# Performance work log

Hardware: AMD Instinct MI355X
Metric: run time of the kernel (lower is better)

Reference implementation:

```python
import jax, jax.numpy as jnp
import numpy as np

H, W, NC, L = 768, 768, 1, 8
PROJ = L * (L + 1) // 2  # = l*(l-1)/2 + l = 36
LMBDA = 0.1
NU = 0.01
SIGMAP = 1.0 / (3.0 + L)
SIGMAS = 1.0
TAUU = 1.0 / 6.0
N_ITERS = 2  # two primal-dual iterations of run()'s hot loop


def _member_matrix():
    # M[z, K] = 1 iff level z lies in combination K=(k1,k2), k1<=z<=k2.
    # Equivalent to the precomputed k_indices lists in k_indices_for_mu().
    M = np.zeros((L, PROJ), dtype=np.float32)
    K = 0
    for k1 in range(L):
        for k2 in range(k1, L):
            M[k1:k2 + 1, K] = 1.0
            K += 1
    return jnp.asarray(M)

_M = _member_matrix()
_K_OVER_L = jnp.arange(1, L + 1, dtype=jnp.float32) / L  # k/l, k = 1..L


def _fwd_diff(x, axis):
    # torch.cat((torch.diff(x, dim=axis), zeros_like(last slice)), dim=axis)
    pad = [(0, 0)] * x.ndim
    pad[axis] = (0, 1)
    return jnp.pad(jnp.diff(x, axis=axis), pad)


def _div(p, axis):
    # Negative adjoint of _fwd_diff (backward difference with the last
    # slice of p treated as zero): (div p)_j = p_j - p_{j-1}.
    n = p.shape[axis]
    sl = [slice(None)] * p.ndim
    sl[axis] = slice(0, n - 1)
    zpad = [(0, 0)] * p.ndim
    zpad[axis] = (0, 1)
    p_eff = jnp.pad(p[tuple(sl)], zpad)
    spad = [(0, 0)] * p.ndim
    spad[axis] = (1, 0)
    sl2 = [slice(None)] * p.ndim
    sl2[axis] = slice(0, n)
    return p_eff - jnp.pad(p_eff, spad)[tuple(sl2)]


def _parabola(ubar, p1, p2, p3, mu1, mu2, f):
    u1 = _fwd_diff(ubar, 0)
    u2 = _fwd_diff(ubar, 1)
    u3 = _fwd_diff(ubar, 3)
    # level-wise gather-sum over combinations via membership matrix
    mu1sum = jnp.einsum('hwcp,zp->hwcz', mu1, _M)
    mu2sum = jnp.einsum('hwcp,zp->hwcz', mu2, _M)
    u1 = p1 + SIGMAP * (u1 + mu1sum)
    u2 = p2 + SIGMAP * (u2 + mu2sum)
    u3 = p3 + SIGMAP * u3
    quad = LMBDA * (_K_OVER_L - f[..., None]) ** 2      # [h,w,c,L]
    B = 0.25 * (u1 * u1 + u2 * u2) - quad
    mask = u3 < B
    # cubic-root solve projecting onto the parabola
    y = u3 + quad
    norm = jnp.sqrt(u1 * u1 + u2 * u2)
    a = 0.5 * norm                      # 2*0.25*norm
    b = (2.0 / 3.0) * (1.0 - 0.5 * y)   # 2/3*(1 - 2*0.25*y)
    sb = jnp.sqrt(jnp.maximum(-b, 0.0))
    d = jnp.where(b < 0, (a - sb ** 3) * (a + sb ** 3), a * a + b ** 3)
    sd = jnp.sqrt(jnp.maximum(d, 0.0))
    c = jnp.cbrt(a + sd)
    c_safe = jnp.where(c == 0, 1.0, c)
    sb3 = jnp.where(sb > 0, sb ** 3, 1.0)
    cosarg = jnp.clip(a / sb3, -1.0, 1.0)
    v_neg = 2.0 * sb * jnp.cos(jnp.arccos(cosarg) / 3.0)
    v = jnp.where((d >= 0) & (c == 0), 0.0,
                  jnp.where(d < 0, v_neg, c - b / c_safe))
    norm_safe = jnp.where(norm == 0, 1.0, norm)
    scale = (v / 0.5) / norm_safe       # v / (2*0.25) / norm
    p1n = jnp.where(mask, jnp.where(norm == 0, 0.0, scale * u1), u1)
    p2n = jnp.where(mask, jnp.where(norm == 0, 0.0, scale * u2), u2)
    p3n = jnp.where(mask, 0.25 * (p1n * p1n + p2n * p2n) - quad, u3)
    return p1n, p2n, p3n


def _l2projection(s1, s2, mubar1, mubar2):
    m1 = s1 - SIGMAS * mubar1
    m2 = s2 - SIGMAS * mubar2
    norm = jnp.sqrt(m1 * m1 + m2 * m2)
    mask = norm > NU
    ns = jnp.where(mask, norm, 1.0)
    return jnp.where(mask, m1 * NU / ns, m1), jnp.where(mask, m2 * NU / ns, m2)


def _mu(mu1, mu2, s1, s2, p1, p2):
    tau = 1.0 / (2.0 + PROJ / 4.0)
    # t[K] = sum of p over levels k1..k2 for combination K (same membership M)
    t1 = jnp.einsum('hwcz,zp->hwcp', p1, _M)
    t2 = jnp.einsum('hwcz,zp->hwcp', p2, _M)
    mu1n = mu1 + tau * (s1 - t1)
    mu2n = mu2 + tau * (s2 - t2)
    return mu1n, mu2n, 2.0 * mu1n - mu1, 2.0 * mu2n - mu2


def _clipping(u, p1, p2, p3):
    div = _div(p1, 0) + _div(p2, 1) + _div(p3, 3)
    un = jnp.clip(u + TAUU * div, 0.0, 1.0)
    return un, 2.0 * un - u


def setup_inputs() -> dict:
    key = jax.random.key(0)
    ks = jax.random.split(key, 12)
    lvl = (H, W, NC, L)
    prj = (H, W, NC, PROJ)
    return {
        'u': jax.random.uniform(ks[0], lvl, jnp.float32),
        'ubar': jax.random.uniform(ks[1], lvl, jnp.float32),
        'p1': jax.random.normal(ks[2], lvl, jnp.float32),
        'p2': jax.random.normal(ks[3], lvl, jnp.float32),
        'p3': jax.random.normal(ks[4], lvl, jnp.float32),
        's1': jax.random.normal(ks[5], prj, jnp.float32),
        's2': jax.random.normal(ks[6], prj, jnp.float32),
        'mu1': jax.random.normal(ks[7], prj, jnp.float32),
        'mu2': jax.random.normal(ks[8], prj, jnp.float32),
        'mubar1': jax.random.normal(ks[9], prj, jnp.float32),
        'mubar2': jax.random.normal(ks[10], prj, jnp.float32),
        'f': jax.random.uniform(ks[11], (H, W, NC), jnp.float32),
    }


def reference(u, ubar, p1, p2, p3, s1, s2, mu1, mu2, mubar1, mubar2, f):
    for _ in range(N_ITERS):
        p1, p2, p3 = _parabola(ubar, p1, p2, p3, mu1, mu2, f)
        s1, s2 = _l2projection(s1, s2, mubar1, mubar2)
        mu1, mu2, mubar1, mubar2 = _mu(mu1, mu2, s1, s2, p1, p2)
        u, ubar = _clipping(u, p1, p2, p3)
    return u
```

## Files before the change

kernel.cpp:

```cpp
#include <hip/hip_runtime.h>
#include <math.h>

#define HH   768
#define WW   768
#define LL   8
#define NPIX (HH*WW)
#define NLVL (NPIX*LL)
#define BLK  128
#define THR  512
#define REC  37

#define SIGMAP (1.0f/11.0f)
#define TAUMU  (1.0f/11.0f)
#define TAUU   (1.0f/6.0f)
#define LMBDA  0.1f
#define NUC    0.01f

__device__ __forceinline__ float4 ld4(const float* p){ return *reinterpret_cast<const float4*>(p); }
__device__ __forceinline__ void  st4(float* p, float4 v){ *reinterpret_cast<float4*>(p) = v; }
__device__ __forceinline__ float2 ld2(const float* p){ return *reinterpret_cast<const float2*>(p); }
__device__ __forceinline__ void  st2(float* p, float2 v){ *reinterpret_cast<float2*>(p) = v; }

__device__ __forceinline__ void parabola1(float u1, float u2, float u3, float quad,
                                          float& p1n, float& p2n, float& p3n)
{
  float nn = u1*u1 + u2*u2;
  float Bv = 0.25f*nn - quad;
  if (u3 < Bv) {
    float y    = u3 + quad;
    float norm = sqrtf(nn);
    float a    = 0.5f*norm;
    float b    = (2.0f/3.0f)*(1.0f - 0.5f*y);
    float sb   = sqrtf(fmaxf(-b, 0.0f));
    float sb3  = sb*sb*sb;
    float d    = (b < 0.0f) ? (a - sb3)*(a + sb3) : (a*a + b*b*b);
    float v;
    if (d < 0.0f) {
      float sb3s = (sb > 0.0f) ? sb3 : 1.0f;
      float ca   = fminf(fmaxf(a/sb3s, -1.0f), 1.0f);
      v = 2.0f*sb*cosf(acosf(ca)*(1.0f/3.0f));
    } else {
      float sd = sqrtf(d);
      float c  = cbrtf(a + sd);
      v = (c == 0.0f) ? 0.0f : (c - b/c);
    }
    float nsafe = (norm == 0.0f) ? 1.0f : norm;
    float scale = (v + v)/nsafe;
    p1n = (norm == 0.0f) ? 0.0f : scale*u1;
    p2n = (norm == 0.0f) ? 0.0f : scale*u2;
    p3n = 0.25f*(p1n*p1n + p2n*p2n) - quad;
  } else {
    p1n = u1; p2n = u2; p3n = u3;
  }
}

__device__ __forceinline__ void stage1_512(const float* __restrict__ g, float* __restrict__ lds, int tid)
{
  #pragma unroll
  for (int j = 0; j < 2; ++j) {
    int g4 = (tid + THR*j) * 4;
    float4 v = ld4(g + g4);
    int pl  = g4 / 36;
    int off = g4 - pl*36;
    float* d = lds + pl*REC + off;
    d[0]=v.x; d[1]=v.y; d[2]=v.z; d[3]=v.w;
  }
  if (tid < 128) {
    int g4 = (tid + 1024) * 4;
    float4 v = ld4(g + g4);
    int pl  = g4 / 36;
    int off = g4 - pl*36;
    float* d = lds + pl*REC + off;
    d[0]=v.x; d[1]=v.y; d[2]=v.z; d[3]=v.w;
  }
}

__device__ __forceinline__ void stage_diff_512(const float* __restrict__ ga, const float* __restrict__ gb,
                                               float* __restrict__ lds, int tid)
{
  #pragma unroll
  for (int j = 0; j < 2; ++j) {
    int g4 = (tid + THR*j) * 4;
    float4 a = ld4(ga + g4);
    float4 b = ld4(gb + g4);
    int pl  = g4 / 36;
    int off = g4 - pl*36;
    float* d = lds + pl*REC + off;
    d[0]=a.x-b.x; d[1]=a.y-b.y; d[2]=a.z-b.z; d[3]=a.w-b.w;
  }
  if (tid < 128) {
    int g4 = (tid + 1024) * 4;
    float4 a = ld4(ga + g4);
    float4 b = ld4(gb + g4);
    int pl  = g4 / 36;
    int off = g4 - pl*36;
    float* d = lds + pl*REC + off;
    d[0]=a.x-b.x; d[1]=a.y-b.y; d[2]=a.z-b.z; d[3]=a.w-b.w;
  }
}

template<int ZB>
__device__ __forceinline__ void memb_scan2(const float* __restrict__ rA, const float* __restrict__ rB,
                                           float (&ms1)[2], float (&ms2)[2])
{
  int K = 0;
  #pragma unroll
  for (int k1 = 0; k1 < 8; ++k1) {
    #pragma unroll
    for (int k2 = k1; k2 < 8; ++k2) {
      if (k2 >= ZB && k1 <= ZB + 1) {
        float v1 = rA[K], v2 = rB[K];
        #pragma unroll
        for (int z = (k1 > ZB ? k1 : ZB); z <= (k2 < ZB+1 ? k2 : ZB+1); ++z) {
          ms1[z-ZB] += v1; ms2[z-ZB] += v2;
        }
      }
      ++K;
    }
  }
}

template<int ZB>
__device__ __forceinline__ void proj_scan2(const float* __restrict__ rA, const float* __restrict__ rB,
                                           const float (&pre1)[9], const float (&pre2)[9],
                                           float (&A1)[2], float (&A2)[2])
{
  int K = 0;
  #pragma unroll
  for (int k1 = 0; k1 < 8; ++k1) {
    #pragma unroll
    for (int k2 = k1; k2 < 8; ++k2) {
      if (k2 >= ZB && k1 <= ZB + 1) {
        float m1 = rA[K], m2 = rB[K];
        float nrm = sqrtf(m1*m1 + m2*m2);
        float s1n, s2n;
        if (nrm > NUC) { float r = NUC/nrm; s1n = m1*r; s2n = m2*r; }
        else           { s1n = m1; s2n = m2; }
        float d1 = s1n - (pre1[k2+1] - pre1[k1]);
        float d2 = s2n - (pre2[k2+1] - pre2[k1]);
        #pragma unroll
        for (int z = (k1 > ZB ? k1 : ZB); z <= (k2 < ZB+1 ? k2 : ZB+1); ++z) {
          A1[z-ZB] += d1; A2[z-ZB] += d2;
        }
      }
      ++K;
    }
  }
}

__global__ __launch_bounds__(THR, 8) void k_iter1(
  const float* __restrict__ ubar, const float* __restrict__ p1,
  const float* __restrict__ p2,   const float* __restrict__ p3,
  const float* __restrict__ s1,   const float* __restrict__ s2,
  const float* __restrict__ mu1,  const float* __restrict__ mu2,
  const float* __restrict__ mb1,  const float* __restrict__ mb2,
  const float* __restrict__ f,
  float* __restrict__ op1, float* __restrict__ op2, float* __restrict__ op3,
  float* __restrict__ oms1, float* __restrict__ oms2)
{
  __shared__ float sA[BLK*REC];
  __shared__ float sB[BLK*REC];

  const int tid  = threadIdx.x;
  const int lpx  = tid & 127;
  const int hi   = tid >> 7;
  const int zb   = hi * 2;
  const int blk0 = blockIdx.x * BLK;
  const int p    = blk0 + lpx;
  const int w  = p % WW;
  const int h  = p / WW;
  const int pr = (w < WW-1) ? p+1  : p;
  const int pd = (h < HH-1) ? p+WW : p;

  stage1_512(mu1 + (size_t)blk0*36, sA, tid);
  stage1_512(mu2 + (size_t)blk0*36, sB, tid);
  __syncthreads();

  const float* rA = sA + lpx*REC;
  const float* rB = sB + lpx*REC;
  float ms1[2] = {0.f,0.f}, ms2[2] = {0.f,0.f};
  switch (hi) {
    case 0: memb_scan2<0>(rA, rB, ms1, ms2); break;
    case 1: memb_scan2<2>(rA, rB, ms1, ms2); break;
    case 2: memb_scan2<4>(rA, rB, ms1, ms2); break;
    default: memb_scan2<6>(rA, rB, ms1, ms2); break;
  }

  float2 ubq  = ld2(ubar + (size_t)p *8 + zb);
  float  ubx  = (zb < 6) ? ubar[(size_t)p*8 + zb + 2] : 0.f;
  float2 ubrq = ld2(ubar + (size_t)pr*8 + zb);
  float2 ubdq = ld2(ubar + (size_t)pd*8 + zb);
  float2 p1q  = ld2(p1 + (size_t)p*8 + zb);
  float2 p2q  = ld2(p2 + (size_t)p*8 + zb);
  float2 p3q  = ld2(p3 + (size_t)p*8 + zb);
  const float fv = f[p];

  float ubv[3]  = {ubq.x, ubq.y, ubx};
  float ubrv[2] = {ubrq.x, ubrq.y};
  float ubdv[2] = {ubdq.x, ubdq.y};
  float p1v[2]  = {p1q.x, p1q.y};
  float p2v[2]  = {p2q.x, p2q.y};
  float p3v[2]  = {p3q.x, p3q.y};

  float pn1[2], pn2[2], pn3[2];
  #pragma unroll
  for (int i = 0; i < 2; ++i) {
    int z = zb + i;
    float du1 = ubdv[i] - ubv[i];
    float du2 = ubrv[i] - ubv[i];
    float du3 = (z < 7) ? (ubv[i+1] - ubv[i]) : 0.f;
    float u1 = p1v[i] + SIGMAP*(du1 + ms1[i]);
    float u2 = p2v[i] + SIGMAP*(du2 + ms2[i]);
    float u3 = p3v[i] + SIGMAP*du3;
    float t  = (float)(z+1)*0.125f - fv;
    float quad = LMBDA*t*t;
    parabola1(u1,u2,u3,quad, pn1[i],pn2[i],pn3[i]);
  }
  st2(op1 + (size_t)p*8 + zb, make_float2(pn1[0],pn1[1]));
  st2(op2 + (size_t)p*8 + zb, make_float2(pn2[0],pn2[1]));
  st2(op3 + (size_t)p*8 + zb, make_float2(pn3[0],pn3[1]));

  __syncthreads();
  float* ex1 = sA;
  float* ex2 = sA + 8*BLK;
  #pragma unroll
  for (int i = 0; i < 2; ++i) {
    ex1[(zb+i)*BLK + lpx] = pn1[i];
    ex2[(zb+i)*BLK + lpx] = pn2[i];
  }
  __syncthreads();
  float pre1[9], pre2[9];
  pre1[0] = 0.f; pre2[0] = 0.f;
  #pragma unroll
  for (int z = 0; z < 8; ++z) {
    pre1[z+1] = pre1[z] + ex1[z*BLK + lpx];
    pre2[z+1] = pre2[z] + ex2[z*BLK + lpx];
  }

  __syncthreads();
  stage_diff_512(s1 + (size_t)blk0*36, mb1 + (size_t)blk0*36, sA, tid);
  stage_diff_512(s2 + (size_t)blk0*36, mb2 + (size_t)blk0*36, sB, tid);
  __syncthreads();

  float A1[2] = {0.f,0.f}, A2[2] = {0.f,0.f};
  switch (hi) {
    case 0: proj_scan2<0>(rA, rB, pre1, pre2, A1, A2); break;
    case 1: proj_scan2<2>(rA, rB, pre1, pre2, A1, A2); break;
    case 2: proj_scan2<4>(rA, rB, pre1, pre2, A1, A2); break;
    default: proj_scan2<6>(rA, rB, pre1, pre2, A1, A2); break;
  }

  st2(oms1 + (size_t)p*8 + zb,
      make_float2(ms1[0] + TAUMU*A1[0], ms1[1] + TAUMU*A1[1]));
  st2(oms2 + (size_t)p*8 + zb,
      make_float2(ms2[0] + TAUMU*A2[0], ms2[1] + TAUMU*A2[1]));
}

__global__ __launch_bounds__(256, 8) void k_parab2(
  const float* __restrict__ ubar,
  float* __restrict__ p1, float* __restrict__ p2, float* __restrict__ p3,
  const float* __restrict__ ms1g, const float* __restrict__ ms2g,
  const float* __restrict__ f)
{
  const int t  = blockIdx.x*blockDim.x + threadIdx.x;
  const int p  = t >> 1;
  const int hi = t & 1;
  const int zb = hi * 4;
  const int w  = p % WW;
  const int h  = p / WW;
  const int pr = (w < WW-1) ? p+1  : p;
  const int pd = (h < HH-1) ? p+WW : p;

  float4 ubq  = ld4(ubar + (size_t)p *8 + zb);
  float  ubx  = hi ? 0.f : ubar[(size_t)p*8 + 4];
  float4 ubrq = ld4(ubar + (size_t)pr*8 + zb);
  float4 ubdq = ld4(ubar + (size_t)pd*8 + zb);
  float4 p1q  = ld4(p1 + (size_t)p*8 + zb);
  float4 p2q  = ld4(p2 + (size_t)p*8 + zb);
  float4 p3q  = ld4(p3 + (size_t)p*8 + zb);
  float4 m1q  = ld4(ms1g + (size_t)p*8 + zb);
  float4 m2q  = ld4(ms2g + (size_t)p*8 + zb);
  const float fv = f[p];

  float ubv[5]  = {ubq.x, ubq.y, ubq.z, ubq.w, ubx};
  float ubrv[4] = {ubrq.x, ubrq.y, ubrq.z, ubrq.w};
  float ubdv[4] = {ubdq.x, ubdq.y, ubdq.z, ubdq.w};
  float p1v[4]  = {p1q.x, p1q.y, p1q.z, p1q.w};
  float p2v[4]  = {p2q.x, p2q.y, p2q.z, p2q.w};
  float p3v[4]  = {p3q.x, p3q.y, p3q.z, p3q.w};
  float ms1[4]  = {m1q.x, m1q.y, m1q.z, m1q.w};
  float ms2[4]  = {m2q.x, m2q.y, m2q.z, m2q.w};

  float pn1[4], pn2[4], pn3[4];
  #pragma unroll
  for (int i = 0; i < 4; ++i) {
    int z = zb + i;
    float du1 = ubdv[i] - ubv[i];
    float du2 = ubrv[i] - ubv[i];
    float du3 = (z < 7) ? (ubv[i+1] - ubv[i]) : 0.f;
    float u1 = p1v[i] + SIGMAP*(du1 + ms1[i]);
    float u2 = p2v[i] + SIGMAP*(du2 + ms2[i]);
    float u3 = p3v[i] + SIGMAP*du3;
    float tt = (float)(z+1)*0.125f - fv;
    float quad = LMBDA*tt*tt;
    parabola1(u1,u2,u3,quad, pn1[i],pn2[i],pn3[i]);
  }
  st4(p1 + (size_t)p*8 + zb, make_float4(pn1[0],pn1[1],pn1[2],pn1[3]));
  st4(p2 + (size_t)p*8 + zb, make_float4(pn2[0],pn2[1],pn2[2],pn2[3]));
  st4(p3 + (size_t)p*8 + zb, make_float4(pn3[0],pn3[1],pn3[2],pn3[3]));
}

__global__ __launch_bounds__(256, 8) void k_clip(
  const float* __restrict__ uin,
  const float* __restrict__ p1, const float* __restrict__ p2,
  const float* __restrict__ p3,
  float* __restrict__ uout, float* __restrict__ ubarout)
{
  const int t  = blockIdx.x*blockDim.x + threadIdx.x;
  const int p  = t >> 1;
  const int hi = t & 1;
  const int zb = hi * 4;
  const int w  = p % WW;
  const int h  = p / WW;
  const int pu = (h > 0) ? p-WW : p;
  const int pl = (w > 0) ? p-1  : p;

  float4 uq   = ld4(uin + (size_t)p *8 + zb);
  float4 a1q  = ld4(p1  + (size_t)p *8 + zb);
  float4 a1uq = ld4(p1  + (size_t)pu*8 + zb);
  float4 a2q  = ld4(p2  + (size_t)p *8 + zb);
  float4 a2lq = ld4(p2  + (size_t)pl*8 + zb);
  float4 a3q  = ld4(p3  + (size_t)p *8 + zb);
  float  a3m  = hi ? p3[(size_t)p*8 + 3] : 0.f;

  float uv[4]  = {uq.x, uq.y, uq.z, uq.w};
  float a1[4]  = {a1q.x, a1q.y, a1q.z, a1q.w};
  float a1u[4] = {a1uq.x, a1uq.y, a1uq.z, a1uq.w};
  float a2[4]  = {a2q.x, a2q.y, a2q.z, a2q.w};
  float a2l[4] = {a2lq.x, a2lq.y, a2lq.z, a2lq.w};
  float a3[4]  = {a3q.x, a3q.y, a3q.z, a3q.w};

  const float fh1 = (h < HH-1) ? 1.f : 0.f;
  const float fh0 = (h > 0)    ? 1.f : 0.f;
  const float fw1 = (w < WW-1) ? 1.f : 0.f;
  const float fw0 = (w > 0)    ? 1.f : 0.f;

  float un[4], ubn[4];
  #pragma unroll
  for (int i = 0; i < 4; ++i) {
    int z = zb + i;
    float d1 = fh1*a1[i] - fh0*a1u[i];
    float d2 = fw1*a2[i] - fw0*a2l[i];
    float upper = (z < 7) ? a3[i] : 0.f;
    float lower = (z > 0) ? ((i > 0) ? a3[i-1] : a3m) : 0.f;
    float d3 = upper - lower;
    float x  = uv[i] + TAUU*(d1+d2+d3);
    x = fminf(fmaxf(x, 0.f), 1.f);
    un[i]  = x;
    ubn[i] = 2.f*x - uv[i];
  }
  st4(uout + (size_t)p*8 + zb, make_float4(un[0],un[1],un[2],un[3]));
  if (ubarout) st4(ubarout + (size_t)p*8 + zb, make_float4(ubn[0],ubn[1],ubn[2],ubn[3]));
}

extern "C" void kernel_launch(void* const* d_in, const int* in_sizes, int n_in,
                              void* d_out, int out_size, void* d_ws, size_t ws_size,
                              hipStream_t stream)
{
  const float* u    = (const float*)d_in[0];
  const float* ubar = (const float*)d_in[1];
  const float* p1   = (const float*)d_in[2];
  const float* p2   = (const float*)d_in[3];
  const float* p3   = (const float*)d_in[4];
  const float* s1   = (const float*)d_in[5];
  const float* s2   = (const float*)d_in[6];
  const float* mu1  = (const float*)d_in[7];
  const float* mu2  = (const float*)d_in[8];
  const float* mb1  = (const float*)d_in[9];
  const float* mb2  = (const float*)d_in[10];
  const float* f    = (const float*)d_in[11];

  float* ws   = (float*)d_ws;
  float* wp1  = ws;
  float* wp2  = ws + 1*(size_t)NLVL;
  float* wp3  = ws + 2*(size_t)NLVL;
  float* wms1 = ws + 3*(size_t)NLVL;
  float* wms2 = ws + 4*(size_t)NLVL;
  float* wub  = ws + 5*(size_t)NLVL;
  float* uo   = (float*)d_out;

  k_iter1 <<<dim3(NPIX/BLK), dim3(THR), 0, stream>>>(
      ubar,p1,p2,p3,s1,s2,mu1,mu2,mb1,mb2,f, wp1,wp2,wp3,wms1,wms2);
  k_clip  <<<dim3(NPIX*2/256), dim3(256), 0, stream>>>(u, wp1,wp2,wp3, uo, wub);
  k_parab2<<<dim3(NPIX*2/256), dim3(256), 0, stream>>>(wub, wp1,wp2,wp3, wms1,wms2, f);
  k_clip  <<<dim3(NPIX*2/256), dim3(256), 0, stream>>>(uo, wp1,wp2,wp3, uo, nullptr);
}
```

Baseline: 627.8 us.

## Shrink k_iter1 blocks and time-share one LDS buffer across mu/s channels

Restructures k_iter1 from 128-pixel/512-thread blocks to 64-pixel/128-thread blocks, each thread handling 4 levels instead of 2. It uses a single LDS buffer reused sequentially for mu1 then mu2, and for the projected s1 then s2. The L2 projection of s onto the nu-ball moves into the staging step, so each combination's norm is computed while loading rather than during the scan. This cuts LDS use per block to raise occupancy. In exchange it loads s1/s2/mubar twice, recomputes the norm, and adds more barriers.

```diff
diff --git a/kernel.cpp b/kernel.cpp
--- a/kernel.cpp
+++ b/kernel.cpp
@@ -6,8 +6,8 @@
 #define LL   8
 #define NPIX (HH*WW)
 #define NLVL (NPIX*LL)
-#define BLK  128
-#define THR  512
+#define BLKI 64
+#define THRI 128
 #define REC  37
 
 #define SIGMAP (1.0f/11.0f)
@@ -18,8 +18,6 @@
 
 __device__ __forceinline__ float4 ld4(const float* p){ return *reinterpret_cast<const float4*>(p); }
 __device__ __forceinline__ void  st4(float* p, float4 v){ *reinterpret_cast<float4*>(p) = v; }
-__device__ __forceinline__ float2 ld2(const float* p){ return *reinterpret_cast<const float2*>(p); }
-__device__ __forceinline__ void  st2(float* p, float2 v){ *reinterpret_cast<float2*>(p) = v; }
 
 __device__ __forceinline__ void parabola1(float u1, float u2, float u3, float quad,
                                           float& p1n, float& p2n, float& p3n)
@@ -54,19 +52,19 @@
   }
 }
 
-__device__ __forceinline__ void stage1_512(const float* __restrict__ g, float* __restrict__ lds, int tid)
-{
-  #pragma unroll
-  for (int j = 0; j < 2; ++j) {
-    int g4 = (tid + THR*j) * 4;
+__device__ __forceinline__ void stage1_128(const float* __restrict__ g, float* __restrict__ lds, int tid)
+{
+  #pragma unroll
+  for (int j = 0; j < 4; ++j) {
+    int g4 = (tid + THRI*j) * 4;
     float4 v = ld4(g + g4);
     int pl  = g4 / 36;
     int off = g4 - pl*36;
     float* d = lds + pl*REC + off;
     d[0]=v.x; d[1]=v.y; d[2]=v.z; d[3]=v.w;
   }
-  if (tid < 128) {
-    int g4 = (tid + 1024) * 4;
+  if (tid < 64) {
+    int g4 = (tid + 512) * 4;
     float4 v = ld4(g + g4);
     int pl  = g4 / 36;
     int off = g4 - pl*36;
@@ -75,45 +73,60 @@
   }
 }
 
-__device__ __forceinline__ void stage_diff_512(const float* __restrict__ ga, const float* __restrict__ gb,
-                                               float* __restrict__ lds, int tid)
-{
-  #pragma unroll
-  for (int j = 0; j < 2; ++j) {
-    int g4 = (tid + THR*j) * 4;
-    float4 a = ld4(ga + g4);
-    float4 b = ld4(gb + g4);
+template<int SEL>
+__device__ __forceinline__ float celem(float m1, float m2)
+{
+  float nrm = sqrtf(m1*m1 + m2*m2);
+  float o = (SEL == 0) ? m1 : m2;
+  if (nrm > NUC) o = o * (NUC/nrm);
+  return o;
+}
+
+template<int SEL>
+__device__ __forceinline__ void stage_c(const float* __restrict__ ga1, const float* __restrict__ gb1,
+                                        const float* __restrict__ ga2, const float* __restrict__ gb2,
+                                        float* __restrict__ lds, int tid)
+{
+  #pragma unroll
+  for (int j = 0; j < 4; ++j) {
+    int g4 = (tid + THRI*j) * 4;
+    float4 a1 = ld4(ga1 + g4), b1 = ld4(gb1 + g4);
+    float4 a2 = ld4(ga2 + g4), b2 = ld4(gb2 + g4);
     int pl  = g4 / 36;
     int off = g4 - pl*36;
     float* d = lds + pl*REC + off;
-    d[0]=a.x-b.x; d[1]=a.y-b.y; d[2]=a.z-b.z; d[3]=a.w-b.w;
-  }
-  if (tid < 128) {
-    int g4 = (tid + 1024) * 4;
-    float4 a = ld4(ga + g4);
-    float4 b = ld4(gb + g4);
+    d[0] = celem<SEL>(a1.x-b1.x, a2.x-b2.x);
+    d[1] = celem<SEL>(a1.y-b1.y, a2.y-b2.y);
+    d[2] = celem<SEL>(a1.z-b1.z, a2.z-b2.z);
+    d[3] = celem<SEL>(a1.w-b1.w, a2.w-b2.w);
+  }
+  if (tid < 64) {
+    int g4 = (tid + 512) * 4;
+    float4 a1 = ld4(ga1 + g4), b1 = ld4(gb1 + g4);
+    float4 a2 = ld4(ga2 + g4), b2 = ld4(gb2 + g4);
     int pl  = g4 / 36;
     int off = g4 - pl*36;
     float* d = lds + pl*REC + off;
-    d[0]=a.x-b.x; d[1]=a.y-b.y; d[2]=a.z-b.z; d[3]=a.w-b.w;
+    d[0] = celem<SEL>(a1.x-b1.x, a2.x-b2.x);
+    d[1] = celem<SEL>(a1.y-b1.y, a2.y-b2.y);
+    d[2] = celem<SEL>(a1.z-b1.z, a2.z-b2.z);
+    d[3] = celem<SEL>(a1.w-b1.w, a2.w-b2.w);
   }
 }
 
 template<int ZB>
-__device__ __forceinline__ void memb_scan2(const float* __restrict__ rA, const float* __restrict__ rB,
-                                           float (&ms1)[2], float (&ms2)[2])
+__device__ __forceinline__ void memb_scan1(const float* __restrict__ r, float (&ms)[4])
 {
   int K = 0;
   #pragma unroll
   for (int k1 = 0; k1 < 8; ++k1) {
     #pragma unroll
     for (int k2 = k1; k2 < 8; ++k2) {
-      if (k2 >= ZB && k1 <= ZB + 1) {
-        float v1 = rA[K], v2 = rB[K];
+      if (k2 >= ZB && k1 < ZB + 4) {
+        float v = r[K];
         #pragma unroll
-        for (int z = (k1 > ZB ? k1 : ZB); z <= (k2 < ZB+1 ? k2 : ZB+1); ++z) {
-          ms1[z-ZB] += v1; ms2[z-ZB] += v2;
-        }
+        for (int z = (k1 > ZB ? k1 : ZB); z <= (k2 < ZB+3 ? k2 : ZB+3); ++z)
+          ms[z-ZB] += v;
       }
       ++K;
     }
@@ -121,34 +134,26 @@
 }
 
 template<int ZB>
-__device__ __forceinline__ void proj_scan2(const float* __restrict__ rA, const float* __restrict__ rB,
-                                           const float (&pre1)[9], const float (&pre2)[9],
-                                           float (&A1)[2], float (&A2)[2])
+__device__ __forceinline__ void projA_scan(const float* __restrict__ r, const float (&pre)[9],
+                                           float (&A)[4])
 {
   int K = 0;
   #pragma unroll
   for (int k1 = 0; k1 < 8; ++k1) {
     #pragma unroll
     for (int k2 = k1; k2 < 8; ++k2) {
-      if (k2 >= ZB && k1 <= ZB + 1) {
-        float m1 = rA[K], m2 = rB[K];
-        float nrm = sqrtf(m1*m1 + m2*m2);
-        float s1n, s2n;
-        if (nrm > NUC) { float r = NUC/nrm; s1n = m1*r; s2n = m2*r; }
-        else           { s1n = m1; s2n = m2; }
-        float d1 = s1n - (pre1[k2+1] - pre1[k1]);
-        float d2 = s2n - (pre2[k2+1] - pre2[k1]);
+      if (k2 >= ZB && k1 < ZB + 4) {
+        float d = r[K] - (pre[k2+1] - pre[k1]);
         #pragma unroll
-        for (int z = (k1 > ZB ? k1 : ZB); z <= (k2 < ZB+1 ? k2 : ZB+1); ++z) {
-          A1[z-ZB] += d1; A2[z-ZB] += d2;
-        }
+        for (int z = (k1 > ZB ? k1 : ZB); z <= (k2 < ZB+3 ? k2 : ZB+3); ++z)
+          A[z-ZB] += d;
       }
       ++K;
     }
   }
 }
 
-__global__ __launch_bounds__(THR, 8) void k_iter1(
+__global__ __launch_bounds__(THRI, 8) void k_iter1(
   const float* __restrict__ ubar, const float* __restrict__ p1,
   const float* __restrict__ p2,   const float* __restrict__ p3,
   const float* __restrict__ s1,   const float* __restrict__ s2,
@@ -158,53 +163,49 @@
   float* __restrict__ op1, float* __restrict__ op2, float* __restrict__ op3,
   float* __restrict__ oms1, float* __restrict__ oms2)
 {
-  __shared__ float sA[BLK*REC];
-  __shared__ float sB[BLK*REC];
+  __shared__ float sBuf[BLKI*REC];
 
   const int tid  = threadIdx.x;
-  const int lpx  = tid & 127;
-  const int hi   = tid >> 7;
-  const int zb   = hi * 2;
-  const int blk0 = blockIdx.x * BLK;
+  const int lpx  = tid & 63;
+  const int hi   = tid >> 6;
+  const int zb   = hi * 4;
+  const int blk0 = blockIdx.x * BLKI;
   const int p    = blk0 + lpx;
   const int w  = p % WW;
   const int h  = p / WW;
   const int pr = (w < WW-1) ? p+1  : p;
   const int pd = (h < HH-1) ? p+WW : p;
 
-  stage1_512(mu1 + (size_t)blk0*36, sA, tid);
-  stage1_512(mu2 + (size_t)blk0*36, sB, tid);
-  __syncthreads();
-
-  const float* rA = sA + lpx*REC;
-  const float* rB = sB + lpx*REC;
-  float ms1[2] = {0.f,0.f}, ms2[2] = {0.f,0.f};
-  switch (hi) {
-    case 0: memb_scan2<0>(rA, rB, ms1, ms2); break;
-    case 1: memb_scan2<2>(rA, rB, ms1, ms2); break;
-    case 2: memb_scan2<4>(rA, rB, ms1, ms2); break;
-    default: memb_scan2<6>(rA, rB, ms1, ms2); break;
-  }
-
-  float2 ubq  = ld2(ubar + (size_t)p *8 + zb);
-  float  ubx  = (zb < 6) ? ubar[(size_t)p*8 + zb + 2] : 0.f;
-  float2 ubrq = ld2(ubar + (size_t)pr*8 + zb);
-  float2 ubdq = ld2(ubar + (size_t)pd*8 + zb);
-  float2 p1q  = ld2(p1 + (size_t)p*8 + zb);
-  float2 p2q  = ld2(p2 + (size_t)p*8 + zb);
-  float2 p3q  = ld2(p3 + (size_t)p*8 + zb);
+  stage1_128(mu1 + (size_t)blk0*36, sBuf, tid);
+  __syncthreads();
+  const float* rC = sBuf + lpx*REC;
+  float ms1[4] = {0.f,0.f,0.f,0.f};
+  if (hi) memb_scan1<4>(rC, ms1); else memb_scan1<0>(rC, ms1);
+  __syncthreads();
+  stage1_128(mu2 + (size_t)blk0*36, sBuf, tid);
+  __syncthreads();
+  float ms2[4] = {0.f,0.f,0.f,0.f};
+  if (hi) memb_scan1<4>(rC, ms2); else memb_scan1<0>(rC, ms2);
+
+  float4 ubq  = ld4(ubar + (size_t)p *8 + zb);
+  float  ubx  = hi ? 0.f : ubar[(size_t)p*8 + 4];
+  float4 ubrq = ld4(ubar + (size_t)pr*8 + zb);
+  float4 ubdq = ld4(ubar + (size_t)pd*8 + zb);
+  float4 p1q  = ld4(p1 + (size_t)p*8 + zb);
+  float4 p2q  = ld4(p2 + (size_t)p*8 + zb);
+  float4 p3q  = ld4(p3 + (size_t)p*8 + zb);
   const float fv = f[p];
 
-  float ubv[3]  = {ubq.x, ubq.y, ubx};
-  float ubrv[2] = {ubrq.x, ubrq.y};
-  float ubdv[2] = {ubdq.x, ubdq.y};
-  float p1v[2]  = {p1q.x, p1q.y};
-  float p2v[2]  = {p2q.x, p2q.y};
-  float p3v[2]  = {p3q.x, p3q.y};
-
-  float pn1[2], pn2[2], pn3[2];
-  #pragma unroll
-  for (int i = 0; i < 2; ++i) {
+  float ubv[5]  = {ubq.x, ubq.y, ubq.z, ubq.w, ubx};
+  float ubrv[4] = {ubrq.x, ubrq.y, ubrq.z, ubrq.w};
+  float ubdv[4] = {ubdq.x, ubdq.y, ubdq.z, ubdq.w};
+  float p1v[4]  = {p1q.x, p1q.y, p1q.z, p1q.w};
+  float p2v[4]  = {p2q.x, p2q.y, p2q.z, p2q.w};
+  float p3v[4]  = {p3q.x, p3q.y, p3q.z, p3q.w};
+
+  float pn1[4], pn2[4], pn3[4];
+  #pragma unroll
+  for (int i = 0; i < 4; ++i) {
     int z = zb + i;
     float du1 = ubdv[i] - ubv[i];
     float du2 = ubrv[i] - ubv[i];
@@ -216,44 +217,46 @@
     float quad = LMBDA*t*t;
     parabola1(u1,u2,u3,quad, pn1[i],pn2[i],pn3[i]);
   }
-  st2(op1 + (size_t)p*8 + zb, make_float2(pn1[0],pn1[1]));
-  st2(op2 + (size_t)p*8 + zb, make_float2(pn2[0],pn2[1]));
-  st2(op3 + (size_t)p*8 + zb, make_float2(pn3[0],pn3[1]));
-
-  __syncthreads();
-  float* ex1 = sA;
-  float* ex2 = sA + 8*BLK;
-  #pragma unroll
-  for (int i = 0; i < 2; ++i) {
-    ex1[(zb+i)*BLK + lpx] = pn1[i];
-    ex2[(zb+i)*BLK + lpx] = pn2[i];
+  st4(op1 + (size_t)p*8 + zb, make_float4(pn1[0],pn1[1],pn1[2],pn1[3]));
+  st4(op2 + (size_t)p*8 + zb, make_float4(pn2[0],pn2[1],pn2[2],pn2[3]));
+  st4(op3 + (size_t)p*8 + zb, make_float4(pn3[0],pn3[1],pn3[2],pn3[3]));
+
+  __syncthreads();
+  float* ex1 = sBuf;
+  float* ex2 = sBuf + 8*BLKI;
+  #pragma unroll
+  for (int i = 0; i < 4; ++i) {
+    ex1[(zb+i)*BLKI + lpx] = pn1[i];
+    ex2[(zb+i)*BLKI + lpx] = pn2[i];
   }
   __syncthreads();
   float pre1[9], pre2[9];
   pre1[0] = 0.f; pre2[0] = 0.f;
   #pragma unroll
   for (int z = 0; z < 8; ++z) {
-    pre1[z+1] = pre1[z] + ex1[z*BLK + lpx];
-    pre2[z+1] = pre2[z] + ex2[z*BLK + lpx];
-  }
-
-  __syncthreads();
-  stage_diff_512(s1 + (size_t)blk0*36, mb1 + (size_t)blk0*36, sA, tid);
-  stage_diff_512(s2 + (size_t)blk0*36, mb2 + (size_t)blk0*36, sB, tid);
-  __syncthreads();
-
-  float A1[2] = {0.f,0.f}, A2[2] = {0.f,0.f};
-  switch (hi) {
-    case 0: proj_scan2<0>(rA, rB, pre1, pre2, A1, A2); break;
-    case 1: proj_scan2<2>(rA, rB, pre1, pre2, A1, A2); break;
-    case 2: proj_scan2<4>(rA, rB, pre1, pre2, A1, A2); break;
-    default: proj_scan2<6>(rA, rB, pre1, pre2, A1, A2); break;
-  }
-
-  st2(oms1 + (size_t)p*8 + zb,
-      make_float2(ms1[0] + TAUMU*A1[0], ms1[1] + TAUMU*A1[1]));
-  st2(oms2 + (size_t)p*8 + zb,
-      make_float2(ms2[0] + TAUMU*A2[0], ms2[1] + TAUMU*A2[1]));
+    pre1[z+1] = pre1[z] + ex1[z*BLKI + lpx];
+    pre2[z+1] = pre2[z] + ex2[z*BLKI + lpx];
+  }
+
+  __syncthreads();
+  stage_c<0>(s1 + (size_t)blk0*36, mb1 + (size_t)blk0*36,
+             s2 + (size_t)blk0*36, mb2 + (size_t)blk0*36, sBuf, tid);
+  __syncthreads();
+  float A1[4] = {0.f,0.f,0.f,0.f};
+  if (hi) projA_scan<4>(rC, pre1, A1); else projA_scan<0>(rC, pre1, A1);
+  __syncthreads();
+  stage_c<1>(s1 + (size_t)blk0*36, mb1 + (size_t)blk0*36,
+             s2 + (size_t)blk0*36, mb2 + (size_t)blk0*36, sBuf, tid);
+  __syncthreads();
+  float A2[4] = {0.f,0.f,0.f,0.f};
+  if (hi) projA_scan<4>(rC, pre2, A2); else projA_scan<0>(rC, pre2, A2);
+
+  st4(oms1 + (size_t)p*8 + zb,
+      make_float4(ms1[0] + TAUMU*A1[0], ms1[1] + TAUMU*A1[1],
+                  ms1[2] + TAUMU*A1[2], ms1[3] + TAUMU*A1[3]));
+  st4(oms2 + (size_t)p*8 + zb,
+      make_float4(ms2[0] + TAUMU*A2[0], ms2[1] + TAUMU*A2[1],
+                  ms2[2] + TAUMU*A2[2], ms2[3] + TAUMU*A2[3]));
 }
 
 __global__ __launch_bounds__(256, 8) void k_parab2(
@@ -389,7 +392,7 @@
   float* wub  = ws + 5*(size_t)NLVL;
   float* uo   = (float*)d_out;
 
-  k_iter1 <<<dim3(NPIX/BLK), dim3(THR), 0, stream>>>(
+  k_iter1 <<<dim3(NPIX/BLKI), dim3(THRI), 0, stream>>>(
       ubar,p1,p2,p3,s1,s2,mu1,mu2,mb1,mb2,f, wp1,wp2,wp3,wms1,wms2);
   k_clip  <<<dim3(NPIX*2/256), dim3(256), 0, stream>>>(u, wp1,wp2,wp3, uo, wub);
   k_parab2<<<dim3(NPIX*2/256), dim3(256), 0, stream>>>(wub, wp1,wp2,wp3, wms1,wms2, f);
```

Result: no change. 638.5 us (+1.7%).
